# Performance work log

Hardware: AMD Instinct MI355X
Metric: run time of the kernel (lower is better)

Reference implementation:

```python
import jax, jax.numpy as jnp
import numpy as np

N_NODES = 50000
N_EDGES = 400000
DIMS = [128, 256, 512, 256, 64, 2]


def setup_inputs() -> dict:
    key = jax.random.key(0)
    ks = jax.random.split(key, 16)
    x = jax.random.normal(ks[0], (N_NODES, DIMS[0]), dtype=jnp.float32)
    edge_index = jax.random.randint(ks[1], (2, N_EDGES), 0, N_NODES, dtype=jnp.int64)
    inp = {"x": x, "edge_index": edge_index}
    for i in range(5):
        fan_in, fan_out = DIMS[i], DIMS[i + 1]
        scale = (2.0 / (fan_in + fan_out)) ** 0.5  # glorot-ish
        inp[f"W{i+1}"] = jax.random.normal(ks[2 + 2 * i], (fan_in, fan_out), dtype=jnp.float32) * scale
        inp[f"b{i+1}"] = jnp.zeros((fan_out,), dtype=jnp.float32)
    return inp


def _gcn_norm(edge_index, n):
    # add self-loops, compute symmetric normalization D^{-1/2} A_hat D^{-1/2}
    loop = jnp.arange(n, dtype=edge_index.dtype)
    src = jnp.concatenate([edge_index[0], loop])
    dst = jnp.concatenate([edge_index[1], loop])
    deg = jax.ops.segment_sum(jnp.ones_like(dst, dtype=jnp.float32), dst, num_segments=n)
    dinv = jnp.where(deg > 0, jax.lax.rsqrt(deg), 0.0)
    norm = dinv[src] * dinv[dst]  # [E+N]
    return src, dst, norm


def _gcn_conv(h, W, b, src, dst, norm, n):
    h = h @ W                                   # [N, out]
    msg = h[src] * norm[:, None]                # gather + scale, [E+N, out]
    out = jax.ops.segment_sum(msg, dst, num_segments=n)  # scatter-add
    return out + b


def reference(x, edge_index, W1, b1, W2, b2, W3, b3, W4, b4, W5, b5):
    n = x.shape[0]
    src, dst, norm = _gcn_norm(edge_index, n)
    h = jax.nn.relu(_gcn_conv(x, W1, b1, src, dst, norm, n))
    h = jax.nn.relu(_gcn_conv(h, W2, b2, src, dst, norm, n))
    h = jax.nn.relu(_gcn_conv(h, W3, b3, src, dst, norm, n))
    h = jax.nn.relu(_gcn_conv(h, W4, b4, src, dst, norm, n))
    h = _gcn_conv(h, W5, b5, src, dst, norm, n)
    return jax.nn.log_softmax(h, axis=1)
```

## Files before the change

kernel.cpp:

```cpp
#include <hip/hip_runtime.h>
#include <math.h>

#define N_NODES 50000
#define N_EDGES 400000

typedef __bf16 bf16x8 __attribute__((ext_vector_type(8)));
typedef float f32x4 __attribute__((ext_vector_type(4)));

__device__ __forceinline__ unsigned bf16_rne(float v) {
    unsigned u = __float_as_uint(v);
    return (u + 0x7FFFu + ((u >> 16) & 1u)) >> 16;
}
__device__ __forceinline__ unsigned pack_split(float v) {
    unsigned hi = bf16_rne(v);
    float hif = __uint_as_float(hi << 16);
    unsigned lo = bf16_rne(v - hif);
    return (hi << 16) | lo;
}
__device__ __forceinline__ float unpack_ps(unsigned w) {
    return __uint_as_float(w & 0xFFFF0000u) + __uint_as_float(w << 16);
}

__global__ void k_zero_i(int* __restrict__ p, int n) {
    int i = blockIdx.x * blockDim.x + threadIdx.x;
    if (i < n) p[i] = 0;
}

__global__ void k_count(const int* __restrict__ dst, int* __restrict__ cnt) {
    int e = blockIdx.x * blockDim.x + threadIdx.x;
    if (e < N_EDGES) atomicAdd(&cnt[dst[e]], 1);
}

__global__ __launch_bounds__(1024) void k_scan(const int* __restrict__ cnt,
                                               int* __restrict__ rowptr,
                                               float* __restrict__ dinv, int n) {
    __shared__ int sm[1024];
    __shared__ int carry;
    if (threadIdx.x == 0) carry = 0;
    __syncthreads();
    for (int base = 0; base < n; base += 1024) {
        int i = base + threadIdx.x;
        int v = (i < n) ? cnt[i] : 0;
        sm[threadIdx.x] = v;
        __syncthreads();
        for (int off = 1; off < 1024; off <<= 1) {
            int t = (threadIdx.x >= (unsigned)off) ? sm[threadIdx.x - off] : 0;
            __syncthreads();
            sm[threadIdx.x] += t;
            __syncthreads();
        }
        if (i < n) {
            rowptr[i] = carry + sm[threadIdx.x] - v;
            dinv[i] = rsqrtf((float)(v + 1));
        }
        __syncthreads();
        if (threadIdx.x == 0) carry += sm[1023];
        __syncthreads();
    }
    if (threadIdx.x == 0) rowptr[n] = carry;
}

__global__ void k_copy_i(const int* __restrict__ s, int* __restrict__ d, int n) {
    int i = blockIdx.x * blockDim.x + threadIdx.x;
    if (i < n) d[i] = s[i];
}

__global__ void k_fill(const int* __restrict__ src, const int* __restrict__ dst,
                       int* __restrict__ cursor, int* __restrict__ csr) {
    int e = blockIdx.x * blockDim.x + threadIdx.x;
    if (e >= N_EDGES) return;
    int d = dst[e];
    int pos = atomicAdd(&cursor[d], 1);
    csr[pos] = src[e];
}

__global__ void k_wprep(const float* __restrict__ W, unsigned* __restrict__ Wtp, int K, int N) {
    int i = blockIdx.x * blockDim.x + threadIdx.x;
    if (i >= K * N) return;
    int k = i / N, n = i % N;
    Wtp[(size_t)n * K + k] = pack_split(W[i]);
}

__global__ void k_rowscale(const float* __restrict__ x, const float* __restrict__ dinv,
                           float* __restrict__ xs) {
    int idx = blockIdx.x * blockDim.x + threadIdx.x;
    if (idx >= N_NODES * 32) return;
    int i = idx >> 5;
    float4 v = ((const float4*)x)[idx];
    float s = dinv[i];
    v.x *= s; v.y *= s; v.z *= s; v.w *= s;
    ((float4*)xs)[idx] = v;
}

template <int VEC, int MODE, int INP, int OUTP>
__global__ __launch_bounds__(256) void k_agg(
    const void* __restrict__ gv, const int* __restrict__ rowptr,
    const int* __restrict__ csr, const float* __restrict__ dinv,
    const float* __restrict__ bias, void* __restrict__ ov)
{
    constexpr int W = 64 * VEC;
    const int wave = threadIdx.x >> 6, lane = threadIdx.x & 63;
    const int node = blockIdx.x * 4 + wave;
    if (node >= N_NODES) return;
    const int col = lane * VEC;

    float acc[VEC];
#pragma unroll
    for (int v = 0; v < VEC; ++v) acc[v] = 0.f;

    auto fetch_add = [&](int r) {
        if constexpr (INP) {
            const unsigned* p = (const unsigned*)gv + (size_t)r * W + col;
            if constexpr (VEC == 4) {
                uint4 t = *(const uint4*)p;
                acc[0] += unpack_ps(t.x); acc[1] += unpack_ps(t.y);
                acc[2] += unpack_ps(t.z); acc[3] += unpack_ps(t.w);
            } else if constexpr (VEC == 2) {
                uint2 t = *(const uint2*)p;
                acc[0] += unpack_ps(t.x); acc[1] += unpack_ps(t.y);
            } else acc[0] += unpack_ps(*p);
        } else {
            const float* p = (const float*)gv + (size_t)r * W + col;
            if constexpr (VEC == 4) {
                float4 t = *(const float4*)p;
                acc[0] += t.x; acc[1] += t.y; acc[2] += t.z; acc[3] += t.w;
            } else if constexpr (VEC == 2) {
                float2 t = *(const float2*)p;
                acc[0] += t.x; acc[1] += t.y;
            } else acc[0] += *(const float*)p;
        }
    };

    fetch_add(node);
    const int beg = rowptr[node], end = rowptr[node + 1];
    for (int j = beg; j < end; ++j) fetch_add(csr[j]);

    const float sc = dinv[node];
    float r[VEC];
#pragma unroll
    for (int v = 0; v < VEC; ++v) {
        float t = sc * acc[v];
        if (MODE == 1) t = fmaxf(t + bias[col + v], 0.f);
        r[v] = t;
    }
    if constexpr (OUTP) {
        unsigned* po = (unsigned*)ov + (size_t)node * W + col;
        if constexpr (VEC == 4)
            *(uint4*)po = make_uint4(pack_split(r[0]), pack_split(r[1]), pack_split(r[2]), pack_split(r[3]));
        else if constexpr (VEC == 2)
            *(uint2*)po = make_uint2(pack_split(r[0]), pack_split(r[1]));
        else *po = pack_split(r[0]);
    } else {
        float* po = (float*)ov + (size_t)node * W + col;
        if constexpr (VEC == 4) *(float4*)po = make_float4(r[0], r[1], r[2], r[3]);
        else if constexpr (VEC == 2) *(float2*)po = make_float2(r[0], r[1]);
        else *po = r[0];
    }
}

__global__ void k_agg2(const float* __restrict__ g, const int* __restrict__ rowptr,
                       const int* __restrict__ csr, const float* __restrict__ dinv,
                       float* __restrict__ o) {
    int i = blockIdx.x * blockDim.x + threadIdx.x;
    if (i >= N_NODES) return;
    float2 a = *(const float2*)&g[2 * (size_t)i];
    int beg = rowptr[i], end = rowptr[i + 1];
    for (int j = beg; j < end; ++j) {
        int s = csr[j];
        float2 t = *(const float2*)&g[2 * (size_t)s];
        a.x += t.x; a.y += t.y;
    }
    float sc = dinv[i];
    o[2 * (size_t)i + 0] = sc * a.x;
    o[2 * (size_t)i + 1] = sc * a.y;
}

template <int WM, int WN>
__global__ __launch_bounds__(256) void k_gemm_mfma(
    const unsigned* __restrict__ Ap, const unsigned* __restrict__ Wtp,
    const float* __restrict__ dinv, const float* __restrict__ bias,
    unsigned* __restrict__ Gp, int M, int K, int N, int mode)
{
    constexpr int BM = 2 * WM, BN = 2 * WN;
    constexpr int AF = WM / 16, BF = WN / 16;
    __shared__ char lds[(2 * BM + 2 * BN) * 64];
    char* Ahi = lds;
    char* Alo = Ahi + BM * 64;
    char* Bhi = Alo + BM * 64;
    char* Blo = Bhi + BN * 64;

    const int tid = threadIdx.x;
    const int m0 = blockIdx.y * BM;
    const int n0 = blockIdx.x * BN;
    const int wv = tid >> 6, l = tid & 63;
    const int wr = wv >> 1, wc = wv & 1;
    const int lr = l & 15, ls = l >> 4;

    int aoff[AF], boff[BF];
#pragma unroll
    for (int f = 0; f < AF; ++f) {
        int row = wr * WM + f * 16 + lr;
        aoff[f] = (row * 64 + ls * 16) ^ ((row & 7) << 4);
    }
#pragma unroll
    for (int j = 0; j < BF; ++j) {
        int row = wc * WN + j * 16 + lr;
        boff[j] = (row * 64 + ls * 16) ^ ((row & 7) << 4);
    }

    f32x4 acc[AF][BF] = {};

    for (int kt = 0; kt < K; kt += 32) {
        __syncthreads();
#pragma unroll
        for (int p = 0; p < BM / 32; ++p) {
            int c = p * 256 + tid;
            int row = c >> 3, c4 = (c & 7) << 2;
            int grow = m0 + row;
            uint4 w = make_uint4(0u, 0u, 0u, 0u);
            if (grow < M) w = *(const uint4*)&Ap[(size_t)grow * K + kt + c4];
            ushort4 hi, lo;
            hi.x = w.x >> 16; lo.x = w.x & 0xFFFFu;
            hi.y = w.y >> 16; lo.y = w.y & 0xFFFFu;
            hi.z = w.z >> 16; lo.z = w.z & 0xFFFFu;
            hi.w = w.w >> 16; lo.w = w.w & 0xFFFFu;
            int off = (row * 64 + c4 * 2) ^ ((row & 7) << 4);
            *(ushort4*)(Ahi + off) = hi;
            *(ushort4*)(Alo + off) = lo;
        }
#pragma unroll
        for (int p = 0; p < BN / 32; ++p) {
            int c = p * 256 + tid;
            int row = c >> 3, c4 = (c & 7) << 2;
            uint4 w = *(const uint4*)&Wtp[(size_t)(n0 + row) * K + kt + c4];
            ushort4 hi, lo;
            hi.x = w.x >> 16; lo.x = w.x & 0xFFFFu;
            hi.y = w.y >> 16; lo.y = w.y & 0xFFFFu;
            hi.z = w.z >> 16; lo.z = w.z & 0xFFFFu;
            hi.w = w.w >> 16; lo.w = w.w & 0xFFFFu;
            int off = (row * 64 + c4 * 2) ^ ((row & 7) << 4);
            *(ushort4*)(Bhi + off) = hi;
            *(ushort4*)(Blo + off) = lo;
        }
        __syncthreads();

        bf16x8 ah[AF], al[AF], bh[BF], bl[BF];
#pragma unroll
        for (int f = 0; f < AF; ++f) {
            ah[f] = *(const bf16x8*)(Ahi + aoff[f]);
            al[f] = *(const bf16x8*)(Alo + aoff[f]);
        }
#pragma unroll
        for (int j = 0; j < BF; ++j) {
            bh[j] = *(const bf16x8*)(Bhi + boff[j]);
            bl[j] = *(const bf16x8*)(Blo + boff[j]);
        }
#pragma unroll
        for (int f = 0; f < AF; ++f)
#pragma unroll
            for (int j = 0; j < BF; ++j) {
                acc[f][j] = __builtin_amdgcn_mfma_f32_16x16x32_bf16(ah[f], bh[j], acc[f][j], 0, 0, 0);
                acc[f][j] = __builtin_amdgcn_mfma_f32_16x16x32_bf16(ah[f], bl[j], acc[f][j], 0, 0, 0);
                acc[f][j] = __builtin_amdgcn_mfma_f32_16x16x32_bf16(al[f], bh[j], acc[f][j], 0, 0, 0);
            }
    }

#pragma unroll
    for (int f = 0; f < AF; ++f)
#pragma unroll
        for (int j = 0; j < BF; ++j) {
            int col = n0 + wc * WN + j * 16 + lr;
            float bc = (mode >= 1) ? bias[col] : 0.f;
#pragma unroll
            for (int reg = 0; reg < 4; ++reg) {
                int r = m0 + wr * WM + f * 16 + ls * 4 + reg;
                if (r < M) {
                    float t = acc[f][j][reg];
                    if (mode == 0)      t = dinv[r] * t;
                    else if (mode == 1) t = fmaxf(t + bc, 0.f);
                    else                t = dinv[r] * fmaxf(t + bc, 0.f);
                    Gp[(size_t)r * N + col] = pack_split(t);
                }
            }
        }
}

__global__ void k_gemm2(const float* __restrict__ A, const float* __restrict__ W,
                        const float* __restrict__ dinv, float* __restrict__ G, int M, int K)
{
    int i = blockIdx.x * blockDim.x + threadIdx.x;
    if (i >= M) return;
    float a0 = 0.f, a1 = 0.f;
    for (int k = 0; k < K; k += 4) {
        float4 a = *(const float4*)&A[(size_t)i * K + k];
        a0 += a.x * W[(k + 0) * 2 + 0] + a.y * W[(k + 1) * 2 + 0]
            + a.z * W[(k + 2) * 2 + 0] + a.w * W[(k + 3) * 2 + 0];
        a1 += a.x * W[(k + 0) * 2 + 1] + a.y * W[(k + 1) * 2 + 1]
            + a.z * W[(k + 2) * 2 + 1] + a.w * W[(k + 3) * 2 + 1];
    }
    float s = dinv[i];
    G[2 * (size_t)i + 0] = s * a0;
    G[2 * (size_t)i + 1] = s * a1;
}

__global__ void k_final(const float* __restrict__ lg, const float* __restrict__ bias,
                        float* __restrict__ out, int M)
{
    int i = blockIdx.x * blockDim.x + threadIdx.x;
    if (i >= M) return;
    float o0 = lg[2 * (size_t)i + 0] + bias[0];
    float o1 = lg[2 * (size_t)i + 1] + bias[1];
    float m = fmaxf(o0, o1);
    float lse = m + logf(expf(o0 - m) + expf(o1 - m));
    out[2 * (size_t)i + 0] = o0 - lse;
    out[2 * (size_t)i + 1] = o1 - lse;
}

extern "C" void kernel_launch(void* const* d_in, const int* in_sizes, int n_in,
                              void* d_out, int out_size, void* d_ws, size_t ws_size,
                              hipStream_t stream) {
    const float* x   = (const float*)d_in[0];
    const int*   ei  = (const int*)d_in[1];
    const int*   src = ei;
    const int*   dst = ei + N_EDGES;
    const float* W1 = (const float*)d_in[2];  const float* b1 = (const float*)d_in[3];
    const float* W2 = (const float*)d_in[4];  const float* b2 = (const float*)d_in[5];
    const float* W3 = (const float*)d_in[6];  const float* b3 = (const float*)d_in[7];
    const float* W4 = (const float*)d_in[8];  const float* b4 = (const float*)d_in[9];
    const float* W5 = (const float*)d_in[10]; const float* b5 = (const float*)d_in[11];
    float* out = (float*)d_out;

    char* ws = (char*)d_ws;
    float*    dinv   = (float*)(ws + 0);
    int*      cnt    = (int*)(ws + 256 * 1024);
    int*      rowptr = (int*)(ws + 512 * 1024);
    int*      cursor = (int*)(ws + 768 * 1024);
    int*      csr    = (int*)(ws + 1024 * 1024);
    unsigned* wt1 = (unsigned*)(ws + 3 * 1024 * 1024);
    unsigned* wt2 = wt1 + 128 * 256;
    unsigned* wt3 = wt2 + 256 * 512;
    unsigned* wt4 = wt3 + 512 * 256;

    char* D = ws + 6 * 1024 * 1024;
    float*    xs   = (float*)D;
    unsigned* aggx = (unsigned*)(D + (size_t)N_NODES * 128 * 4);
    unsigned* h1s  = (unsigned*)(D + (size_t)N_NODES * 512 * 4);
    unsigned* a2   = (unsigned*)(D + (size_t)N_NODES * 768 * 4);
    unsigned* h2   = (unsigned*)D;
    unsigned* g3s  = h1s;
    unsigned* h3   = a2;
    unsigned* g4s  = (unsigned*)D;
    float*    h4   = (float*)(D + (size_t)N_NODES * 64 * 4);
    float*    g5s  = (float*)(D + (size_t)N_NODES * 128 * 4);
    float*    lgt  = (float*)(D + (size_t)N_NODES * 132 * 4);

    const int T = 256;
    const int nodeB = (N_NODES + T - 1) / T;
    const int edgeB = (N_EDGES + T - 1) / T;
    const int aggB  = (N_NODES + 3) / 4;
    const int gy    = (N_NODES + 63) / 64;

    k_zero_i<<<nodeB, T, 0, stream>>>(cnt, N_NODES);
    k_count<<<edgeB, T, 0, stream>>>(dst, cnt);
    k_scan<<<1, 1024, 0, stream>>>(cnt, rowptr, dinv, N_NODES);
    k_copy_i<<<nodeB, T, 0, stream>>>(rowptr, cursor, N_NODES);
    k_fill<<<edgeB, T, 0, stream>>>(src, dst, cursor, csr);
    k_wprep<<<(128 * 256 + T - 1) / T, T, 0, stream>>>(W1, wt1, 128, 256);
    k_wprep<<<(256 * 512 + T - 1) / T, T, 0, stream>>>(W2, wt2, 256, 512);
    k_wprep<<<(512 * 256 + T - 1) / T, T, 0, stream>>>(W3, wt3, 512, 256);
    k_wprep<<<(256 * 64 + T - 1) / T, T, 0, stream>>>(W4, wt4, 256, 64);

    k_rowscale<<<(N_NODES * 32 + T - 1) / T, T, 0, stream>>>(x, dinv, xs);
    k_agg<2, 0, 0, 1><<<aggB, T, 0, stream>>>(xs, rowptr, csr, dinv, nullptr, aggx);
    k_gemm_mfma<32, 64><<<dim3(2, gy), T, 0, stream>>>(aggx, wt1, dinv, b1, h1s, N_NODES, 128, 256, 2);

    k_agg<4, 0, 1, 1><<<aggB, T, 0, stream>>>(h1s, rowptr, csr, dinv, nullptr, a2);
    k_gemm_mfma<32, 64><<<dim3(4, gy), T, 0, stream>>>(a2, wt2, dinv, b2, h2, N_NODES, 256, 512, 1);

    k_gemm_mfma<32, 64><<<dim3(2, gy), T, 0, stream>>>(h2, wt3, dinv, nullptr, g3s, N_NODES, 512, 256, 0);
    k_agg<4, 1, 1, 1><<<aggB, T, 0, stream>>>(g3s, rowptr, csr, dinv, b3, h3);

    k_gemm_mfma<32, 32><<<dim3(1, gy), T, 0, stream>>>(h3, wt4, dinv, nullptr, g4s, N_NODES, 256, 64, 0);
    k_agg<1, 1, 1, 0><<<aggB, T, 0, stream>>>(g4s, rowptr, csr, dinv, b4, h4);

    k_gemm2<<<nodeB, T, 0, stream>>>(h4, W5, dinv, g5s, N_NODES, 64);
    k_agg2<<<nodeB, T, 0, stream>>>(g5s, rowptr, csr, dinv, lgt);
    k_final<<<nodeB, T, 0, stream>>>(lgt, b5, out, N_NODES);
}
```

Before: 698.0 us.

## Double-buffer LDS tiles in split-bf16 MFMA GEMM with register prefetch

Restructures the GEMM main loop so the global loads for the next K-tile are issued into registers before the MFMA work on the current tile. They are written to an alternate LDS buffer afterwards, which leaves one barrier per iteration instead of two. The goal is to hide global memory latency behind the matrix-core work. In exchange, LDS use doubles and the prefetch registers raise register pressure, which may lower occupancy.

```diff
diff --git a/kernel.cpp b/kernel.cpp
--- a/kernel.cpp
+++ b/kernel.cpp
@@ -183,11 +183,9 @@
 {
     constexpr int BM = 2 * WM, BN = 2 * WN;
     constexpr int AF = WM / 16, BF = WN / 16;
-    __shared__ char lds[(2 * BM + 2 * BN) * 64];
-    char* Ahi = lds;
-    char* Alo = Ahi + BM * 64;
-    char* Bhi = Alo + BM * 64;
-    char* Blo = Bhi + BN * 64;
+    constexpr int ACH = BM / 32, BCH = BN / 32;
+    constexpr int BUF = (2 * BM + 2 * BN) * 64;
+    __shared__ char lds[2 * BUF];
 
     const int tid = threadIdx.x;
     const int m0 = blockIdx.y * BM;
@@ -208,17 +206,35 @@
         boff[j] = (row * 64 + ls * 16) ^ ((row & 7) << 4);
     }
 
-    f32x4 acc[AF][BF] = {};
-
-    for (int kt = 0; kt < K; kt += 32) {
-        __syncthreads();
-#pragma unroll
-        for (int p = 0; p < BM / 32; ++p) {
+    uint4 ra[ACH], rb[BCH];
+
+    auto issue = [&](int kt) {
+#pragma unroll
+        for (int p = 0; p < ACH; ++p) {
             int c = p * 256 + tid;
             int row = c >> 3, c4 = (c & 7) << 2;
             int grow = m0 + row;
-            uint4 w = make_uint4(0u, 0u, 0u, 0u);
-            if (grow < M) w = *(const uint4*)&Ap[(size_t)grow * K + kt + c4];
+            ra[p] = make_uint4(0u, 0u, 0u, 0u);
+            if (grow < M) ra[p] = *(const uint4*)&Ap[(size_t)grow * K + kt + c4];
+        }
+#pragma unroll
+        for (int p = 0; p < BCH; ++p) {
+            int c = p * 256 + tid;
+            int row = c >> 3, c4 = (c & 7) << 2;
+            rb[p] = *(const uint4*)&Wtp[(size_t)(n0 + row) * K + kt + c4];
+        }
+    };
+
+    auto commit = [&](int buf) {
+        char* Ahi = lds + buf * BUF;
+        char* Alo = Ahi + BM * 64;
+        char* Bhi = Alo + BM * 64;
+        char* Blo = Bhi + BN * 64;
+#pragma unroll
+        for (int p = 0; p < ACH; ++p) {
+            int c = p * 256 + tid;
+            int row = c >> 3, c4 = (c & 7) << 2;
+            uint4 w = ra[p];
             ushort4 hi, lo;
             hi.x = w.x >> 16; lo.x = w.x & 0xFFFFu;
             hi.y = w.y >> 16; lo.y = w.y & 0xFFFFu;
@@ -229,10 +245,10 @@
             *(ushort4*)(Alo + off) = lo;
         }
 #pragma unroll
-        for (int p = 0; p < BN / 32; ++p) {
+        for (int p = 0; p < BCH; ++p) {
             int c = p * 256 + tid;
             int row = c >> 3, c4 = (c & 7) << 2;
-            uint4 w = *(const uint4*)&Wtp[(size_t)(n0 + row) * K + kt + c4];
+            uint4 w = rb[p];
             ushort4 hi, lo;
             hi.x = w.x >> 16; lo.x = w.x & 0xFFFFu;
             hi.y = w.y >> 16; lo.y = w.y & 0xFFFFu;
@@ -242,18 +258,30 @@
             *(ushort4*)(Bhi + off) = hi;
             *(ushort4*)(Blo + off) = lo;
         }
-        __syncthreads();
-
+    };
+
+    f32x4 acc[AF][BF] = {};
+    const int nt = K / 32;
+
+    issue(0);
+    commit(0);
+    __syncthreads();
+    int cur = 0;
+
+    for (int t = 0; t < nt; ++t) {
+        if (t + 1 < nt) issue((t + 1) * 32);
+
+        const char* base = lds + cur * BUF;
         bf16x8 ah[AF], al[AF], bh[BF], bl[BF];
 #pragma unroll
         for (int f = 0; f < AF; ++f) {
-            ah[f] = *(const bf16x8*)(Ahi + aoff[f]);
-            al[f] = *(const bf16x8*)(Alo + aoff[f]);
+            ah[f] = *(const bf16x8*)(base + aoff[f]);
+            al[f] = *(const bf16x8*)(base + BM * 64 + aoff[f]);
         }
 #pragma unroll
         for (int j = 0; j < BF; ++j) {
-            bh[j] = *(const bf16x8*)(Bhi + boff[j]);
-            bl[j] = *(const bf16x8*)(Blo + boff[j]);
+            bh[j] = *(const bf16x8*)(base + 2 * BM * 64 + boff[j]);
+            bl[j] = *(const bf16x8*)(base + 2 * BM * 64 + BN * 64 + boff[j]);
         }
 #pragma unroll
         for (int f = 0; f < AF; ++f)
@@ -263,6 +291,12 @@
                 acc[f][j] = __builtin_amdgcn_mfma_f32_16x16x32_bf16(ah[f], bl[j], acc[f][j], 0, 0, 0);
                 acc[f][j] = __builtin_amdgcn_mfma_f32_16x16x32_bf16(al[f], bh[j], acc[f][j], 0, 0, 0);
             }
+
+        if (t + 1 < nt) {
+            commit(cur ^ 1);
+            __syncthreads();
+            cur ^= 1;
+        }
     }
 
 #pragma unroll
```

Result: no change. 704.3 us (+0.9%).
